# Kernel optimization log

Hardware: AMD Instinct MI355X
Metric: run time of the kernel (lower is better)

The kernel has to match this reference:

```python
import jax, jax.numpy as jnp
import numpy as np
import math

B, T, L, M = 2, 16, 256, 512
D, H, DH, HT, ROT = 1024, 16, 64, 8, 32
EPS = 1e-5
NEG = jnp.float32(-1e9)
SCALE = 1.0 / math.sqrt(DH)


def _ln(x, g, b):
    mu = jnp.mean(x, -1, keepdims=True)
    var = jnp.mean((x - mu) ** 2, -1, keepdims=True)
    return (x - mu) * jax.lax.rsqrt(var + EPS) * g + b


def _rotate_half(x):
    x1, x2 = jnp.split(x, 2, axis=-1)
    return jnp.concatenate([-x2, x1], axis=-1)


def _apply_rope(t, pos):
    # t: (..., DH), pos broadcastable to (..., ROT)
    t_rot, t_pass = t[..., :ROT], t[..., ROT:]
    t_rot = t_rot * jnp.cos(pos) + _rotate_half(t_rot) * jnp.sin(pos)
    return jnp.concatenate([t_rot, t_pass], axis=-1)


def _decoder_layer(x, context, rope,
                   ca_ng, ca_nb, ca_cng, ca_cnb, ca_wq, ca_wkv, ca_wo,
                   ta_ng, ta_nb, ta_wqkv, ta_bqkv, ta_wo,
                   ff_ng, ff_nb, ff_w1, ff_w2,
                   context_mask, attn_mask):
    # ---- CrossAttention over flattened (t l) sequence ----
    xf = x.reshape(B, T * L, D)
    xn = _ln(xf, ca_ng, ca_nb)
    cn = _ln(context, ca_cng, ca_cnb)
    q = (xn @ ca_wq).reshape(B, T * L, H, DH)
    k, v = jnp.split(cn @ ca_wkv, 2, axis=-1)
    k = k.reshape(B, M, H, DH)
    v = v.reshape(B, M, H, DH)
    scores = jnp.einsum('bnhd,bmhd->bhnm', q, k) * SCALE
    scores = jnp.where(context_mask[:, None, None, :], scores, NEG)
    attn = jax.nn.softmax(scores, axis=-1)
    o = jnp.einsum('bhnm,bmhd->bnhd', attn, v).reshape(B, T * L, H * DH)
    x = x + (o @ ca_wo).reshape(B, T, L, D)

    # ---- PatchWiseTemporalAttention: attention over T at each spatial l ----
    xn = _ln(x, ta_ng, ta_nb)
    qkv = xn @ ta_wqkv + ta_bqkv  # (B,T,L,3*HT*DH)
    q, k, v = jnp.split(qkv, 3, axis=-1)
    q = q.reshape(B, T, L, HT, DH)
    k = k.reshape(B, T, L, HT, DH)
    v = v.reshape(B, T, L, HT, DH)
    # varlen rotary: masks are left-aligned so packed position == frame index t
    pos = rope[:, None, None, :]  # (T,1,1,ROT)
    q = _apply_rope(q, pos)
    k = _apply_rope(k, pos)
    scores = jnp.einsum('bqlhd,bklhd->blhqk', q, k) * SCALE
    scores = jnp.where(attn_mask[:, None, None, None, :], scores, NEG)
    attn = jax.nn.softmax(scores, axis=-1)
    o = jnp.einsum('blhqk,bklhd->bqlhd', attn, v).reshape(B, T, L, HT * DH)
    # pad_input fills zeros at invalid (masked) query rows before to_out (no bias)
    o = o * attn_mask[:, :, None, None].astype(o.dtype)
    x = x + o @ ta_wo

    # ---- FeedForward (LN -> Linear -> GELU(exact) -> Linear) ----
    h = jax.nn.gelu(_ln(x, ff_ng, ff_nb) @ ff_w1, approximate=False)
    x = x + h @ ff_w2
    return x


def setup_inputs():
    key = jax.random.key(0)
    ks = jax.random.split(key, 16)
    s = 0.02
    inner, inner_t, hid = H * DH, HT * DH, 4 * D
    lens = jax.random.randint(ks[0], (B,), 2, T + 1)
    attn_mask = jnp.arange(T)[None, :] < lens[:, None]  # left-aligned ragged lengths
    clens = jax.random.randint(ks[1], (B,), M // 2, M + 1)
    context_mask = jnp.arange(M)[None, :] < clens[:, None]
    return dict(
        x=jax.random.normal(ks[2], (B, T, L, D), jnp.float32),
        context=jax.random.normal(ks[3], (B, M, D), jnp.float32),
        rope=jax.random.normal(ks[4], (T, ROT), jnp.float32),
        ca_ng=jnp.ones((D,), jnp.float32), ca_nb=jnp.zeros((D,), jnp.float32),
        ca_cng=jnp.ones((D,), jnp.float32), ca_cnb=jnp.zeros((D,), jnp.float32),
        ca_wq=jax.random.normal(ks[5], (D, inner), jnp.float32) * s,
        ca_wkv=jax.random.normal(ks[6], (D, 2 * inner), jnp.float32) * s,
        ca_wo=jax.random.normal(ks[7], (inner, D), jnp.float32) * s,
        ta_ng=jnp.ones((D,), jnp.float32), ta_nb=jnp.zeros((D,), jnp.float32),
        ta_wqkv=jax.random.normal(ks[8], (D, 3 * inner_t), jnp.float32) * s,
        ta_bqkv=jnp.zeros((3 * inner_t,), jnp.float32),
        ta_wo=jax.random.normal(ks[9], (inner_t, D), jnp.float32) * s,
        ff_ng=jnp.ones((D,), jnp.float32), ff_nb=jnp.zeros((D,), jnp.float32),
        ff_w1=jax.random.normal(ks[10], (D, hid), jnp.float32) * s,
        ff_w2=jax.random.normal(ks[11], (hid, D), jnp.float32) * s,
        context_mask=context_mask,
        attn_mask=attn_mask,
    )


def reference(x, context, rope,
              ca_ng, ca_nb, ca_cng, ca_cnb, ca_wq, ca_wkv, ca_wo,
              ta_ng, ta_nb, ta_wqkv, ta_bqkv, ta_wo,
              ff_ng, ff_nb, ff_w1, ff_w2,
              context_mask, attn_mask):
    return _decoder_layer(x, context, rope,
                          ca_ng, ca_nb, ca_cng, ca_cnb, ca_wq, ca_wkv, ca_wo,
                          ta_ng, ta_nb, ta_wqkv, ta_bqkv, ta_wo,
                          ff_ng, ff_nb, ff_w1, ff_w2,
                          context_mask, attn_mask)
```

## Files before the change

### kernel.cpp

```cpp
#include <hip/hip_runtime.h>
#include <hip/hip_bf16.h>
#include <stdint.h>

#define DEV static __device__ __forceinline__

constexpr int kB = 2, kT = 16, kL = 256, kM = 512;
constexpr int kD = 1024, kH = 16, kDH = 64, kHT = 8, kROT = 32;
constexpr int kN = kT * kL;
constexpr float kEPS = 1e-5f;
constexpr float kNEG = -1.0e9f;
constexpr float kSCALE = 0.125f;

typedef __attribute__((ext_vector_type(8))) short short8;
typedef __attribute__((ext_vector_type(4))) float floatx4;

DEV float b2f(__hip_bfloat16 v) { return __bfloat162float(v); }
DEV __hip_bfloat16 f2b(float v) { return __float2bfloat16(v); }
DEV float s2f(short x) {
  __hip_bfloat16_raw r; r.x = (unsigned short)x;
  return __bfloat162float(__hip_bfloat16(r));
}

DEV void gl2lds16(const __hip_bfloat16* g, __hip_bfloat16* l) {
  __builtin_amdgcn_global_load_lds(
      (const __attribute__((address_space(1))) void*)g,
      (__attribute__((address_space(3))) void*)l, 16, 0, 0);
}

__global__ void mask_convert(const unsigned char* __restrict__ raw, int n,
                             int* __restrict__ out) {
  int i = blockIdx.x * blockDim.x + threadIdx.x;
  if (i >= n) return;
  unsigned char b1 = raw[1], b3 = raw[3];
  int v;
  if (b1 == 0x3F) {
    v = ((const unsigned short*)raw)[i] != 0;
  } else if (b3 == 0x3F) {
    v = ((const float*)raw)[i] != 0.0f;
  } else if (b1 == 1) {
    v = raw[i] != 0;
  } else {
    v = ((const int*)raw)[i] != 0;
  }
  out[i] = v;
}

__global__ __launch_bounds__(256) void transpose_w(
    const float* __restrict__ W, __hip_bfloat16* __restrict__ Wt,
    int Kd, int Nd) {
  __shared__ float tile[32][33];
  int n0 = blockIdx.x * 32, k0 = blockIdx.y * 32;
  int tx = threadIdx.x & 31, ty = threadIdx.x >> 5;
  for (int i = 0; i < 32; i += 8)
    tile[ty + i][tx] = W[(size_t)(k0 + ty + i) * Nd + n0 + tx];
  __syncthreads();
  for (int i = 0; i < 32; i += 8)
    Wt[(size_t)(n0 + ty + i) * Kd + k0 + tx] = f2b(tile[tx][ty + i]);
}

__global__ __launch_bounds__(256) void ln_rows(
    const float* __restrict__ X, const float* __restrict__ g,
    const float* __restrict__ bb, __hip_bfloat16* __restrict__ out) {
  int row = blockIdx.x, tid = threadIdx.x;
  float4 xv = *(const float4*)(X + (size_t)row * kD + tid * 4);
  float s = xv.x + xv.y + xv.z + xv.w;
  float s2 = xv.x * xv.x + xv.y * xv.y + xv.z * xv.z + xv.w * xv.w;
  for (int off = 32; off; off >>= 1) {
    s += __shfl_down(s, off);
    s2 += __shfl_down(s2, off);
  }
  __shared__ float rs[4], rs2[4];
  if ((tid & 63) == 0) { rs[tid >> 6] = s; rs2[tid >> 6] = s2; }
  __syncthreads();
  float ts = rs[0] + rs[1] + rs[2] + rs[3];
  float ts2 = rs2[0] + rs2[1] + rs2[2] + rs2[3];
  float mu = ts * (1.f / kD);
  float var = ts2 * (1.f / kD) - mu * mu;
  float rstd = rsqrtf(var + kEPS);
  float4 gv = *(const float4*)(g + tid * 4);
  float4 bv = *(const float4*)(bb + tid * 4);
  ushort4 o;
  o.x = __hip_bfloat16_raw(f2b((xv.x - mu) * rstd * gv.x + bv.x)).x;
  o.y = __hip_bfloat16_raw(f2b((xv.y - mu) * rstd * gv.y + bv.y)).x;
  o.z = __hip_bfloat16_raw(f2b((xv.z - mu) * rstd * gv.z + bv.z)).x;
  o.w = __hip_bfloat16_raw(f2b((xv.w - mu) * rstd * gv.w + bv.w)).x;
  *(ushort4*)(out + (size_t)row * kD + tid * 4) = o;
}

__global__ __launch_bounds__(256) void gemm_bf16(
    const __hip_bfloat16* __restrict__ A,
    const __hip_bfloat16* __restrict__ Bt,
    const float* __restrict__ bias,
    const float* __restrict__ res,
    int gelu,
    void* __restrict__ out, int outBf16,
    int Md, int Nd, int Kd) {
  __shared__ __align__(16) __hip_bfloat16 As[128 * 32];
  __shared__ __align__(16) __hip_bfloat16 Bs[128 * 32];
  int m0 = blockIdx.x * 128, n0 = blockIdx.y * 128;
  int tid = threadIdx.x, wave = tid >> 6, lane = tid & 63;
  int l16 = lane & 15, quad = lane >> 4;
  int wm = (wave >> 1) * 64, wn = (wave & 1) * 64;

  int srow = wave * 16 + (lane >> 2);
  int scol = (lane & 3) * 8;
  const __hip_bfloat16* Ag0 = A + (size_t)(m0 + srow) * Kd + scol;
  const __hip_bfloat16* Ag1 = A + (size_t)(m0 + 64 + srow) * Kd + scol;
  const __hip_bfloat16* Bg0 = Bt + (size_t)(n0 + srow) * Kd + scol;
  const __hip_bfloat16* Bg1 = Bt + (size_t)(n0 + 64 + srow) * Kd + scol;
  __hip_bfloat16* Al0 = As + wave * 16 * 32;
  __hip_bfloat16* Al1 = As + (64 + wave * 16) * 32;
  __hip_bfloat16* Bl0 = Bs + wave * 16 * 32;
  __hip_bfloat16* Bl1 = Bs + (64 + wave * 16) * 32;

  floatx4 acc[4][4] = {};
  for (int k0 = 0; k0 < Kd; k0 += 32) {
    gl2lds16(Ag0 + k0, Al0);
    gl2lds16(Ag1 + k0, Al1);
    gl2lds16(Bg0 + k0, Bl0);
    gl2lds16(Bg1 + k0, Bl1);
    __syncthreads();
    short8 af[4], bf[4];
    #pragma unroll
    for (int mf = 0; mf < 4; mf++)
      af[mf] = *(const short8*)(&As[(wm + mf * 16 + l16) * 32 + quad * 8]);
    #pragma unroll
    for (int nf = 0; nf < 4; nf++)
      bf[nf] = *(const short8*)(&Bs[(wn + nf * 16 + l16) * 32 + quad * 8]);
    #pragma unroll
    for (int mf = 0; mf < 4; mf++)
      #pragma unroll
      for (int nf = 0; nf < 4; nf++)
        acc[mf][nf] = __builtin_amdgcn_mfma_f32_16x16x32_bf16(
            af[mf], bf[nf], acc[mf][nf], 0, 0, 0);
    __syncthreads();
  }
  #pragma unroll
  for (int mf = 0; mf < 4; mf++) {
    #pragma unroll
    for (int nf = 0; nf < 4; nf++) {
      int col = n0 + wn + nf * 16 + l16;
      float bv = bias ? bias[col] : 0.f;
      #pragma unroll
      for (int r = 0; r < 4; r++) {
        int row = m0 + wm + mf * 16 + quad * 4 + r;
        float v = acc[mf][nf][r] + bv;
        if (gelu) {
          float z = v * (1.5957691216f + 0.0713548162f * v * v);
          v = v * (1.f / (1.f + __expf(-z)));
        }
        size_t o = (size_t)row * Nd + col;
        if (res) v += res[o];
        if (outBf16) ((__hip_bfloat16*)out)[o] = f2b(v);
        else         ((float*)out)[o] = v;
      }
    }
  }
}

__global__ __launch_bounds__(256) void cross_attn_mfma(
    const __hip_bfloat16* __restrict__ Qb,
    const __hip_bfloat16* __restrict__ KVb,
    const int* __restrict__ cmask,
    __hip_bfloat16* __restrict__ Ob) {
  __shared__ __align__(16) __hip_bfloat16 Vbf[2][8][64][8];
  __shared__ __align__(16) __hip_bfloat16 Paf[4][8][16][8];
  int b = blockIdx.y >> 4, h = blockIdx.y & 15;
  int q0 = blockIdx.x * 64;
  int tid = threadIdx.x, wave = tid >> 6, lane = tid & 63;
  int l16 = lane & 15, quad = lane >> 4;

  const __hip_bfloat16* qrow =
      Qb + (size_t)(b * kN + q0 + wave * 16 + l16) * 1024 + h * 64 + quad * 8;
  short8 qf0 = *(const short8*)qrow;
  short8 qf1 = *(const short8*)(qrow + 32);

  floatx4 of[4] = {};
  float Mr[4] = {-1e30f, -1e30f, -1e30f, -1e30f};
  float Lr[4] = {};

  int skey = tid >> 2, sd0 = (tid & 3) * 16;

  for (int kt = 0; kt < 8; kt++) {
    int buf = kt & 1;
    {
      const __hip_bfloat16* src =
          KVb + (size_t)(b * kM + kt * 64 + skey) * 2048 + 1024 + h * 64 + sd0;
      short8 v0 = *(const short8*)src;
      short8 v1 = *(const short8*)(src + 8);
      int kb = skey >> 3, kj = skey & 7;
      #pragma unroll
      for (int j = 0; j < 8; j++) {
        Vbf[buf][kb][sd0 + j][kj] = __hip_bfloat16(__hip_bfloat16_raw{(unsigned short)v0[j]});
        Vbf[buf][kb][sd0 + 8 + j][kj] = __hip_bfloat16(__hip_bfloat16_raw{(unsigned short)v1[j]});
      }
    }
    __syncthreads();

    floatx4 sf[4];
    #pragma unroll
    for (int nf = 0; nf < 4; nf++) {
      const __hip_bfloat16* krow =
          KVb + (size_t)(b * kM + kt * 64 + nf * 16 + l16) * 2048 + h * 64 + quad * 8;
      short8 kf0 = *(const short8*)krow;
      short8 kf1 = *(const short8*)(krow + 32);
      floatx4 z = {};
      z = __builtin_amdgcn_mfma_f32_16x16x32_bf16(qf0, kf0, z, 0, 0, 0);
      z = __builtin_amdgcn_mfma_f32_16x16x32_bf16(qf1, kf1, z, 0, 0, 0);
      sf[nf] = z;
    }

    float sv[4][4];
    #pragma unroll
    for (int nf = 0; nf < 4; nf++) {
      int mk = cmask[b * kM + kt * 64 + nf * 16 + l16];
      #pragma unroll
      for (int r = 0; r < 4; r++)
        sv[nf][r] = mk ? sf[nf][r] * kSCALE : kNEG;
    }
    float mx[4];
    #pragma unroll
    for (int r = 0; r < 4; r++) {
      float m = fmaxf(fmaxf(sv[0][r], sv[1][r]), fmaxf(sv[2][r], sv[3][r]));
      #pragma unroll
      for (int off = 1; off < 16; off <<= 1) m = fmaxf(m, __shfl_xor(m, off));
      mx[r] = m;
    }
    float alpha[4], Mn[4];
    #pragma unroll
    for (int r = 0; r < 4; r++) {
      Mn[r] = fmaxf(Mr[r], mx[r]);
      alpha[r] = __expf(Mr[r] - Mn[r]);
      Mr[r] = Mn[r];
    }
    float p[4][4];
    float rsum[4];
    #pragma unroll
    for (int r = 0; r < 4; r++) {
      float s = 0.f;
      #pragma unroll
      for (int nf = 0; nf < 4; nf++) {
        float e = __expf(sv[nf][r] - Mn[r]);
        p[nf][r] = e; s += e;
      }
      #pragma unroll
      for (int off = 1; off < 16; off <<= 1) s += __shfl_xor(s, off);
      rsum[r] = s;
    }
    #pragma unroll
    for (int r = 0; r < 4; r++) Lr[r] = Lr[r] * alpha[r] + rsum[r];
    #pragma unroll
    for (int df = 0; df < 4; df++)
      #pragma unroll
      for (int r = 0; r < 4; r++) of[df][r] *= alpha[r];

    #pragma unroll
    for (int nf = 0; nf < 4; nf++) {
      int col = nf * 16 + l16;
      int kb = col >> 3, kj = col & 7;
      #pragma unroll
      for (int r = 0; r < 4; r++)
        Paf[wave][kb][quad * 4 + r][kj] = f2b(p[nf][r]);
    }
    __builtin_amdgcn_s_waitcnt(0);

    short8 pf0 = *(const short8*)(&Paf[wave][quad][l16][0]);
    short8 pf1 = *(const short8*)(&Paf[wave][quad + 4][l16][0]);
    #pragma unroll
    for (int df = 0; df < 4; df++) {
      short8 vf0 = *(const short8*)(&Vbf[buf][quad][df * 16 + l16][0]);
      short8 vf1 = *(const short8*)(&Vbf[buf][quad + 4][df * 16 + l16][0]);
      of[df] = __builtin_amdgcn_mfma_f32_16x16x32_bf16(pf0, vf0, of[df], 0, 0, 0);
      of[df] = __builtin_amdgcn_mfma_f32_16x16x32_bf16(pf1, vf1, of[df], 0, 0, 0);
    }
  }

  #pragma unroll
  for (int df = 0; df < 4; df++) {
    #pragma unroll
    for (int r = 0; r < 4; r++) {
      int row = q0 + wave * 16 + quad * 4 + r;
      float v = of[df][r] / Lr[r];
      Ob[(size_t)(b * kN + row) * 1024 + h * 64 + df * 16 + l16] = f2b(v);
    }
  }
}

__global__ __launch_bounds__(64) void temporal_attn(
    const __hip_bfloat16* __restrict__ QKVb,
    const float* __restrict__ rope,
    const int* __restrict__ amask,
    __hip_bfloat16* __restrict__ Otb) {
  __shared__ float qs[16][65], ks[16][65], vs[16][65];
  __shared__ float Ps[16][17];
  int idx = blockIdx.x;
  int h = idx & 7, l = (idx >> 3) & 255, b = idx >> 11;
  int lane = threadIdx.x;

  {
    int tr = lane >> 2, c0 = (lane & 3) * 16;
    const __hip_bfloat16* base =
        QKVb + ((size_t)(b * kT + tr) * kL + l) * 1536 + h * 64;
    short8 qa = *(const short8*)(base + c0);
    short8 qb = *(const short8*)(base + c0 + 8);
    short8 ka = *(const short8*)(base + 512 + c0);
    short8 kb = *(const short8*)(base + 512 + c0 + 8);
    short8 va = *(const short8*)(base + 1024 + c0);
    short8 vb = *(const short8*)(base + 1024 + c0 + 8);
    #pragma unroll
    for (int j = 0; j < 8; j++) {
      qs[tr][c0 + j] = s2f(qa[j]) * kSCALE;
      qs[tr][c0 + 8 + j] = s2f(qb[j]) * kSCALE;
      ks[tr][c0 + j] = s2f(ka[j]);
      ks[tr][c0 + 8 + j] = s2f(kb[j]);
      vs[tr][c0 + j] = s2f(va[j]);
      vs[tr][c0 + 8 + j] = s2f(vb[j]);
    }
  }
  __syncthreads();
  {
    int rt = lane >> 2, rd0 = (lane & 3) * 8;
    float nq[8], nk[8];
    for (int j = 0; j < 8; j++) {
      int d = rd0 + j;
      float ang = rope[rt * kROT + d];
      float cv = cosf(ang), sv = sinf(ang);
      float oq = (d < 16) ? -qs[rt][d + 16] : qs[rt][d - 16];
      float ok = (d < 16) ? -ks[rt][d + 16] : ks[rt][d - 16];
      nq[j] = qs[rt][d] * cv + oq * sv;
      nk[j] = ks[rt][d] * cv + ok * sv;
    }
    __syncthreads();
    for (int j = 0; j < 8; j++) { qs[rt][rd0 + j] = nq[j]; ks[rt][rd0 + j] = nk[j]; }
  }
  __syncthreads();
  {
    int tq = lane >> 2, tk0 = (lane & 3) * 4;
    float s[4] = {0, 0, 0, 0};
    for (int d = 0; d < 64; d++) {
      float qv = qs[tq][d];
      s[0] += qv * ks[tk0 + 0][d];
      s[1] += qv * ks[tk0 + 1][d];
      s[2] += qv * ks[tk0 + 2][d];
      s[3] += qv * ks[tk0 + 3][d];
    }
    for (int jj = 0; jj < 4; jj++)
      Ps[tq][tk0 + jj] = amask[b * kT + tk0 + jj] ? s[jj] : kNEG;
  }
  __syncthreads();
  if (lane < 16) {
    float mx = -1e30f;
    for (int k = 0; k < 16; k++) mx = fmaxf(mx, Ps[lane][k]);
    float sum = 0.f;
    for (int k = 0; k < 16; k++) { float p = __expf(Ps[lane][k] - mx); Ps[lane][k] = p; sum += p; }
    float inv = 1.f / sum;
    for (int k = 0; k < 16; k++) Ps[lane][k] *= inv;
  }
  __syncthreads();
  for (int tq = 0; tq < 16; tq++) {
    float acc = 0.f;
    for (int tk = 0; tk < 16; tk++) acc += Ps[tq][tk] * vs[tk][lane];
    float qm = amask[b * kT + tq] ? 1.f : 0.f;
    Otb[((size_t)(b * kT + tq) * kL + l) * 512 + h * 64 + lane] = f2b(acc * qm);
  }
}

extern "C" void kernel_launch(void* const* d_in, const int* in_sizes, int n_in,
                              void* d_out, int out_size, void* d_ws, size_t ws_size,
                              hipStream_t stream) {
  const float* x       = (const float*)d_in[0];
  const float* ctx     = (const float*)d_in[1];
  const float* rope    = (const float*)d_in[2];
  const float* ca_ng   = (const float*)d_in[3];
  const float* ca_nb   = (const float*)d_in[4];
  const float* ca_cng  = (const float*)d_in[5];
  const float* ca_cnb  = (const float*)d_in[6];
  const float* ca_wq   = (const float*)d_in[7];
  const float* ca_wkv  = (const float*)d_in[8];
  const float* ca_wo   = (const float*)d_in[9];
  const float* ta_ng   = (const float*)d_in[10];
  const float* ta_nb   = (const float*)d_in[11];
  const float* ta_wqkv = (const float*)d_in[12];
  const float* ta_bqkv = (const float*)d_in[13];
  const float* ta_wo   = (const float*)d_in[14];
  const float* ff_ng   = (const float*)d_in[15];
  const float* ff_nb   = (const float*)d_in[16];
  const float* ff_w1   = (const float*)d_in[17];
  const float* ff_w2   = (const float*)d_in[18];
  const unsigned char* cmraw = (const unsigned char*)d_in[19];
  const unsigned char* amraw = (const unsigned char*)d_in[20];

  char* wsc = (char*)d_ws;
  size_t off = 0;
  auto take = [&](size_t bytes) {
    char* p = wsc + off;
    off = (off + bytes + 255) & ~(size_t)255;
    return p;
  };
  __hip_bfloat16* wqT   = (__hip_bfloat16*)take((size_t)1024 * 1024 * 2);
  __hip_bfloat16* wkvT  = (__hip_bfloat16*)take((size_t)2048 * 1024 * 2);
  __hip_bfloat16* woT   = (__hip_bfloat16*)take((size_t)1024 * 1024 * 2);
  __hip_bfloat16* wqkvT = (__hip_bfloat16*)take((size_t)1536 * 1024 * 2);
  __hip_bfloat16* tawoT = (__hip_bfloat16*)take((size_t)1024 * 512 * 2);
  __hip_bfloat16* ffw1T = (__hip_bfloat16*)take((size_t)4096 * 1024 * 2);
  __hip_bfloat16* ffw2T = (__hip_bfloat16*)take((size_t)1024 * 4096 * 2);
  __hip_bfloat16* XN  = (__hip_bfloat16*)take((size_t)8192 * 1024 * 2);
  __hip_bfloat16* CN  = (__hip_bfloat16*)take((size_t)1024 * 1024 * 2);
  __hip_bfloat16* Qb  = (__hip_bfloat16*)take((size_t)8192 * 1024 * 2);
  __hip_bfloat16* KVb = (__hip_bfloat16*)take((size_t)1024 * 2048 * 2);
  __hip_bfloat16* Ob  = (__hip_bfloat16*)take((size_t)8192 * 1024 * 2);
  float*          X1  = (float*)take((size_t)8192 * 1024 * 4);
  __hip_bfloat16* Hb  = (__hip_bfloat16*)take((size_t)8192 * 4096 * 2);
  int* cmask = (int*)take((size_t)kB * kM * 4);
  int* amask = (int*)take((size_t)kB * kT * 4);
  if (off > ws_size) return;

  __hip_bfloat16* QKVb = Hb;
  __hip_bfloat16* OTb  = Qb;

  auto gemm = [&](const __hip_bfloat16* A, const __hip_bfloat16* Bt,
                  const float* bias, const float* res, int gelu, void* out,
                  int outBf16, int Md, int Nd, int Kd) {
    gemm_bf16<<<dim3(Md / 128, Nd / 128), dim3(256), 0, stream>>>(
        A, Bt, bias, res, gelu, out, outBf16, Md, Nd, Kd);
  };

  mask_convert<<<dim3((kB * kM + 255) / 256), dim3(256), 0, stream>>>(cmraw, kB * kM, cmask);
  mask_convert<<<dim3(1), dim3(256), 0, stream>>>(amraw, kB * kT, amask);
  transpose_w<<<dim3(1024 / 32, 1024 / 32), dim3(256), 0, stream>>>(ca_wq, wqT, 1024, 1024);
  transpose_w<<<dim3(2048 / 32, 1024 / 32), dim3(256), 0, stream>>>(ca_wkv, wkvT, 1024, 2048);
  transpose_w<<<dim3(1024 / 32, 1024 / 32), dim3(256), 0, stream>>>(ca_wo, woT, 1024, 1024);
  transpose_w<<<dim3(1536 / 32, 1024 / 32), dim3(256), 0, stream>>>(ta_wqkv, wqkvT, 1024, 1536);
  transpose_w<<<dim3(1024 / 32, 512 / 32), dim3(256), 0, stream>>>(ta_wo, tawoT, 512, 1024);
  transpose_w<<<dim3(4096 / 32, 1024 / 32), dim3(256), 0, stream>>>(ff_w1, ffw1T, 1024, 4096);
  transpose_w<<<dim3(1024 / 32, 4096 / 32), dim3(256), 0, stream>>>(ff_w2, ffw2T, 4096, 1024);

  ln_rows<<<dim3(8192), dim3(256), 0, stream>>>(x, ca_ng, ca_nb, XN);
  ln_rows<<<dim3(1024), dim3(256), 0, stream>>>(ctx, ca_cng, ca_cnb, CN);
  gemm(XN, wqT, nullptr, nullptr, 0, Qb, 1, 8192, 1024, 1024);
  gemm(CN, wkvT, nullptr, nullptr, 0, KVb, 1, 1024, 2048, 1024);
  cross_attn_mfma<<<dim3(kN / 64, kB * kH), dim3(256), 0, stream>>>(Qb, KVb, cmask, Ob);
  gemm(Ob, woT, nullptr, x, 0, X1, 0, 8192, 1024, 1024);

  ln_rows<<<dim3(8192), dim3(256), 0, stream>>>(X1, ta_ng, ta_nb, XN);
  gemm(XN, wqkvT, ta_bqkv, nullptr, 0, QKVb, 1, 8192, 1536, 1024);
  temporal_attn<<<dim3(kB * kL * kHT), dim3(64), 0, stream>>>(QKVb, rope, amask, OTb);
  gemm(OTb, tawoT, nullptr, X1, 0, X1, 0, 8192, 1024, 512);

  ln_rows<<<dim3(8192), dim3(256), 0, stream>>>(X1, ff_ng, ff_nb, XN);
  gemm(XN, ffw1T, nullptr, nullptr, 1, Hb, 1, 8192, 4096, 1024);
  gemm(Hb, ffw2T, nullptr, X1, 0, d_out, 0, 8192, 1024, 4096);
}
```

Baseline: 707.9 us.

## Batch prep launches, merge LN and QKV GEMMs, widen GEMM K-tile with swizzle

Merges the seven weight transposes and two mask conversions into one launch, and the input and context layernorms into one kernel. It also combines the Q and KV projection GEMMs into a single paired launch. Separately, the GEMM K-tile grows from 32 to 64 with an XOR-swizzled LDS layout to avoid bank conflicts and halve the barrier count. The aim is to cut launch overhead and raise GEMM throughput, at the cost of doubled shared memory per block, which may lower occupancy.

```diff
diff --git a/kernel.cpp b/kernel.cpp
--- a/kernel.cpp
+++ b/kernel.cpp
@@ -27,29 +27,48 @@
       (__attribute__((address_space(3))) void*)l, 16, 0, 0);
 }
 
-__global__ void mask_convert(const unsigned char* __restrict__ raw, int n,
-                             int* __restrict__ out) {
-  int i = blockIdx.x * blockDim.x + threadIdx.x;
-  if (i >= n) return;
+struct TransArgs {
+  const float* src[7];
+  __hip_bfloat16* dst[7];
+  const unsigned char* cmraw;
+  const unsigned char* amraw;
+  int* cmask;
+  int* amask;
+};
+__constant__ const int kTKd[7] = {1024, 1024, 1024, 1024, 512, 1024, 4096};
+__constant__ const int kTNd[7] = {1024, 2048, 1024, 1536, 1024, 4096, 1024};
+__constant__ const int kTCum[8] = {0, 1024, 3072, 4096, 5632, 6144, 10240, 14336};
+
+DEV int mask_val(const unsigned char* raw, int i) {
   unsigned char b1 = raw[1], b3 = raw[3];
-  int v;
-  if (b1 == 0x3F) {
-    v = ((const unsigned short*)raw)[i] != 0;
-  } else if (b3 == 0x3F) {
-    v = ((const float*)raw)[i] != 0.0f;
-  } else if (b1 == 1) {
-    v = raw[i] != 0;
-  } else {
-    v = ((const int*)raw)[i] != 0;
-  }
-  out[i] = v;
-}
-
-__global__ __launch_bounds__(256) void transpose_w(
-    const float* __restrict__ W, __hip_bfloat16* __restrict__ Wt,
-    int Kd, int Nd) {
+  if (b1 == 0x3F) return ((const unsigned short*)raw)[i] != 0;
+  if (b3 == 0x3F) return ((const float*)raw)[i] != 0.0f;
+  if (b1 == 1)    return raw[i] != 0;
+  return ((const int*)raw)[i] != 0;
+}
+
+__global__ __launch_bounds__(256) void transpose_all(TransArgs a) {
+  int id = blockIdx.x;
+  if (id >= 14336) {
+    if (id == 14336) {
+      for (int i = threadIdx.x; i < kB * kM; i += 256)
+        a.cmask[i] = mask_val(a.cmraw, i);
+    } else {
+      if (threadIdx.x < kB * kT)
+        a.amask[threadIdx.x] = mask_val(a.amraw, threadIdx.x);
+    }
+    return;
+  }
+  int seg = 0;
+  #pragma unroll
+  for (int s = 1; s < 7; s++) seg += (id >= kTCum[s]);
+  unsigned t = id - kTCum[seg];
+  int Kd = kTKd[seg], Nd = kTNd[seg];
+  unsigned ntx = Nd / 32;
+  int n0 = (t % ntx) * 32, k0 = (t / ntx) * 32;
+  const float* W = a.src[seg];
+  __hip_bfloat16* Wt = a.dst[seg];
   __shared__ float tile[32][33];
-  int n0 = blockIdx.x * 32, k0 = blockIdx.y * 32;
   int tx = threadIdx.x & 31, ty = threadIdx.x >> 5;
   for (int i = 0; i < 32; i += 8)
     tile[ty + i][tx] = W[(size_t)(k0 + ty + i) * Nd + n0 + tx];
@@ -58,11 +77,9 @@
     Wt[(size_t)(n0 + ty + i) * Kd + k0 + tx] = f2b(tile[tx][ty + i]);
 }
 
-__global__ __launch_bounds__(256) void ln_rows(
-    const float* __restrict__ X, const float* __restrict__ g,
-    const float* __restrict__ bb, __hip_bfloat16* __restrict__ out) {
-  int row = blockIdx.x, tid = threadIdx.x;
-  float4 xv = *(const float4*)(X + (size_t)row * kD + tid * 4);
+DEV void ln_body(const float* xr, const float* g, const float* bb,
+                 __hip_bfloat16* outr, int tid) {
+  float4 xv = *(const float4*)(xr + tid * 4);
   float s = xv.x + xv.y + xv.z + xv.w;
   float s2 = xv.x * xv.x + xv.y * xv.y + xv.z * xv.z + xv.w * xv.w;
   for (int off = 32; off; off >>= 1) {
@@ -84,55 +101,75 @@
   o.y = __hip_bfloat16_raw(f2b((xv.y - mu) * rstd * gv.y + bv.y)).x;
   o.z = __hip_bfloat16_raw(f2b((xv.z - mu) * rstd * gv.z + bv.z)).x;
   o.w = __hip_bfloat16_raw(f2b((xv.w - mu) * rstd * gv.w + bv.w)).x;
-  *(ushort4*)(out + (size_t)row * kD + tid * 4) = o;
-}
-
-__global__ __launch_bounds__(256) void gemm_bf16(
-    const __hip_bfloat16* __restrict__ A,
-    const __hip_bfloat16* __restrict__ Bt,
-    const float* __restrict__ bias,
-    const float* __restrict__ res,
-    int gelu,
-    void* __restrict__ out, int outBf16,
-    int Md, int Nd, int Kd) {
-  __shared__ __align__(16) __hip_bfloat16 As[128 * 32];
-  __shared__ __align__(16) __hip_bfloat16 Bs[128 * 32];
-  int m0 = blockIdx.x * 128, n0 = blockIdx.y * 128;
+  *(ushort4*)(outr + tid * 4) = o;
+}
+
+__global__ __launch_bounds__(256) void ln_rows(
+    const float* __restrict__ X, const float* __restrict__ g,
+    const float* __restrict__ bb, __hip_bfloat16* __restrict__ out) {
+  int row = blockIdx.x;
+  ln_body(X + (size_t)row * kD, g, bb, out + (size_t)row * kD, threadIdx.x);
+}
+
+__global__ __launch_bounds__(256) void ln_rows2(
+    const float* __restrict__ X, const float* __restrict__ g,
+    const float* __restrict__ bb, __hip_bfloat16* __restrict__ out,
+    const float* __restrict__ X2, const float* __restrict__ g2,
+    const float* __restrict__ bb2, __hip_bfloat16* __restrict__ out2) {
+  int row = blockIdx.x;
+  if (row < 8192)
+    ln_body(X + (size_t)row * kD, g, bb, out + (size_t)row * kD, threadIdx.x);
+  else {
+    int r = row - 8192;
+    ln_body(X2 + (size_t)r * kD, g2, bb2, out2 + (size_t)r * kD, threadIdx.x);
+  }
+}
+
+DEV void gemm_body(__hip_bfloat16* As, __hip_bfloat16* Bs,
+                   const __hip_bfloat16* A, const __hip_bfloat16* Bt,
+                   const float* bias, const float* res, int gelu,
+                   void* out, int outBf16, int Nd, int Kd, int m0, int n0) {
   int tid = threadIdx.x, wave = tid >> 6, lane = tid & 63;
   int l16 = lane & 15, quad = lane >> 4;
   int wm = (wave >> 1) * 64, wn = (wave & 1) * 64;
 
-  int srow = wave * 16 + (lane >> 2);
-  int scol = (lane & 3) * 8;
-  const __hip_bfloat16* Ag0 = A + (size_t)(m0 + srow) * Kd + scol;
-  const __hip_bfloat16* Ag1 = A + (size_t)(m0 + 64 + srow) * Kd + scol;
-  const __hip_bfloat16* Bg0 = Bt + (size_t)(n0 + srow) * Kd + scol;
-  const __hip_bfloat16* Bg1 = Bt + (size_t)(n0 + 64 + srow) * Kd + scol;
-  __hip_bfloat16* Al0 = As + wave * 16 * 32;
-  __hip_bfloat16* Al1 = As + (64 + wave * 16) * 32;
-  __hip_bfloat16* Bl0 = Bs + wave * 16 * 32;
-  __hip_bfloat16* Bl1 = Bs + (64 + wave * 16) * 32;
+  int srow = wave * 32 + (lane >> 3);
+  int schunk8 = (((lane & 7) ^ ((lane >> 3) & 7)) << 3);
+  const __hip_bfloat16* Ag = A + (size_t)(m0 + srow) * Kd + schunk8;
+  const __hip_bfloat16* Bg = Bt + (size_t)(n0 + srow) * Kd + schunk8;
+  __hip_bfloat16* Al = As + wave * 32 * 64;
+  __hip_bfloat16* Bl = Bs + wave * 32 * 64;
 
   floatx4 acc[4][4] = {};
-  for (int k0 = 0; k0 < Kd; k0 += 32) {
-    gl2lds16(Ag0 + k0, Al0);
-    gl2lds16(Ag1 + k0, Al1);
-    gl2lds16(Bg0 + k0, Bl0);
-    gl2lds16(Bg1 + k0, Bl1);
+  for (int k0 = 0; k0 < Kd; k0 += 64) {
+    #pragma unroll
+    for (int i = 0; i < 4; i++) {
+      gl2lds16(Ag + (size_t)(i * 8) * Kd + k0, Al + i * 512);
+      gl2lds16(Bg + (size_t)(i * 8) * Kd + k0, Bl + i * 512);
+    }
     __syncthreads();
-    short8 af[4], bf[4];
-    #pragma unroll
-    for (int mf = 0; mf < 4; mf++)
-      af[mf] = *(const short8*)(&As[(wm + mf * 16 + l16) * 32 + quad * 8]);
-    #pragma unroll
-    for (int nf = 0; nf < 4; nf++)
-      bf[nf] = *(const short8*)(&Bs[(wn + nf * 16 + l16) * 32 + quad * 8]);
-    #pragma unroll
-    for (int mf = 0; mf < 4; mf++)
-      #pragma unroll
-      for (int nf = 0; nf < 4; nf++)
-        acc[mf][nf] = __builtin_amdgcn_mfma_f32_16x16x32_bf16(
-            af[mf], bf[nf], acc[mf][nf], 0, 0, 0);
+    #pragma unroll
+    for (int half = 0; half < 2; half++) {
+      short8 af[4], bf4[4];
+      #pragma unroll
+      for (int mf = 0; mf < 4; mf++) {
+        int row = wm + mf * 16 + l16;
+        int phys = (quad + half * 4) ^ (row & 7);
+        af[mf] = *(const short8*)(&As[row * 64 + phys * 8]);
+      }
+      #pragma unroll
+      for (int nf = 0; nf < 4; nf++) {
+        int row = wn + nf * 16 + l16;
+        int phys = (quad + half * 4) ^ (row & 7);
+        bf4[nf] = *(const short8*)(&Bs[row * 64 + phys * 8]);
+      }
+      #pragma unroll
+      for (int mf = 0; mf < 4; mf++)
+        #pragma unroll
+        for (int nf = 0; nf < 4; nf++)
+          acc[mf][nf] = __builtin_amdgcn_mfma_f32_16x16x32_bf16(
+              af[mf], bf4[nf], acc[mf][nf], 0, 0, 0);
+    }
     __syncthreads();
   }
   #pragma unroll
@@ -155,6 +192,34 @@
         else         ((float*)out)[o] = v;
       }
     }
+  }
+}
+
+__global__ __launch_bounds__(256) void gemm_bf16(
+    const __hip_bfloat16* __restrict__ A, const __hip_bfloat16* __restrict__ Bt,
+    const float* __restrict__ bias, const float* __restrict__ res, int gelu,
+    void* __restrict__ out, int outBf16, int Nd, int Kd) {
+  __shared__ __align__(16) __hip_bfloat16 As[128 * 64];
+  __shared__ __align__(16) __hip_bfloat16 Bs[128 * 64];
+  gemm_body(As, Bs, A, Bt, bias, res, gelu, out, outBf16, Nd, Kd,
+            blockIdx.x * 128, blockIdx.y * 128);
+}
+
+__global__ __launch_bounds__(256) void gemm_pair(
+    const __hip_bfloat16* __restrict__ A0, const __hip_bfloat16* __restrict__ B0,
+    void* __restrict__ o0,
+    const __hip_bfloat16* __restrict__ A1, const __hip_bfloat16* __restrict__ B1,
+    void* __restrict__ o1) {
+  __shared__ __align__(16) __hip_bfloat16 As[128 * 64];
+  __shared__ __align__(16) __hip_bfloat16 Bs[128 * 64];
+  int id = blockIdx.x;
+  if (id < 512) {
+    gemm_body(As, Bs, A0, B0, nullptr, nullptr, 0, o0, 1, 1024, 1024,
+              (id & 63) * 128, (id >> 6) * 128);
+  } else {
+    int r = id - 512;
+    gemm_body(As, Bs, A1, B1, nullptr, nullptr, 0, o1, 1, 2048, 1024,
+              (r & 7) * 128, (r >> 3) * 128);
   }
 }
 
@@ -422,23 +487,23 @@
                   const float* bias, const float* res, int gelu, void* out,
                   int outBf16, int Md, int Nd, int Kd) {
     gemm_bf16<<<dim3(Md / 128, Nd / 128), dim3(256), 0, stream>>>(
-        A, Bt, bias, res, gelu, out, outBf16, Md, Nd, Kd);
+        A, Bt, bias, res, gelu, out, outBf16, Nd, Kd);
   };
 
-  mask_convert<<<dim3((kB * kM + 255) / 256), dim3(256), 0, stream>>>(cmraw, kB * kM, cmask);
-  mask_convert<<<dim3(1), dim3(256), 0, stream>>>(amraw, kB * kT, amask);
-  transpose_w<<<dim3(1024 / 32, 1024 / 32), dim3(256), 0, stream>>>(ca_wq, wqT, 1024, 1024);
-  transpose_w<<<dim3(2048 / 32, 1024 / 32), dim3(256), 0, stream>>>(ca_wkv, wkvT, 1024, 2048);
-  transpose_w<<<dim3(1024 / 32, 1024 / 32), dim3(256), 0, stream>>>(ca_wo, woT, 1024, 1024);
-  transpose_w<<<dim3(1536 / 32, 1024 / 32), dim3(256), 0, stream>>>(ta_wqkv, wqkvT, 1024, 1536);
-  transpose_w<<<dim3(1024 / 32, 512 / 32), dim3(256), 0, stream>>>(ta_wo, tawoT, 512, 1024);
-  transpose_w<<<dim3(4096 / 32, 1024 / 32), dim3(256), 0, stream>>>(ff_w1, ffw1T, 1024, 4096);
-  transpose_w<<<dim3(1024 / 32, 4096 / 32), dim3(256), 0, stream>>>(ff_w2, ffw2T, 4096, 1024);
-
-  ln_rows<<<dim3(8192), dim3(256), 0, stream>>>(x, ca_ng, ca_nb, XN);
-  ln_rows<<<dim3(1024), dim3(256), 0, stream>>>(ctx, ca_cng, ca_cnb, CN);
-  gemm(XN, wqT, nullptr, nullptr, 0, Qb, 1, 8192, 1024, 1024);
-  gemm(CN, wkvT, nullptr, nullptr, 0, KVb, 1, 1024, 2048, 1024);
+  TransArgs ta;
+  ta.src[0] = ca_wq;   ta.dst[0] = wqT;
+  ta.src[1] = ca_wkv;  ta.dst[1] = wkvT;
+  ta.src[2] = ca_wo;   ta.dst[2] = woT;
+  ta.src[3] = ta_wqkv; ta.dst[3] = wqkvT;
+  ta.src[4] = ta_wo;   ta.dst[4] = tawoT;
+  ta.src[5] = ff_w1;   ta.dst[5] = ffw1T;
+  ta.src[6] = ff_w2;   ta.dst[6] = ffw2T;
+  ta.cmraw = cmraw; ta.amraw = amraw; ta.cmask = cmask; ta.amask = amask;
+  transpose_all<<<dim3(14338), dim3(256), 0, stream>>>(ta);
+
+  ln_rows2<<<dim3(9216), dim3(256), 0, stream>>>(x, ca_ng, ca_nb, XN,
+                                                 ctx, ca_cng, ca_cnb, CN);
+  gemm_pair<<<dim3(640), dim3(256), 0, stream>>>(XN, wqT, Qb, CN, wkvT, KVb);
   cross_attn_mfma<<<dim3(kN / 64, kB * kH), dim3(256), 0, stream>>>(Qb, KVb, cmask, Ob);
   gemm(Ob, woT, nullptr, x, 0, X1, 0, 8192, 1024, 1024);
 
```

After: 685.7 us. 1.03x faster.
